# Optimization experiments

Hardware: AMD Instinct MI355X
Metric: run time of the kernel (lower is better)

Reference implementation:

```python
import math
import jax, jax.numpy as jnp
import numpy as np

B, C, T = 8, 512, 8192
UP, DOWN, UP_K, DOWN_K = 2, 2, 12, 12


def kaiser_sinc_filter1d(cutoff, half_width, kernel_size):
    even = kernel_size % 2 == 0
    half_size = kernel_size // 2
    delta_f = 4 * half_width
    A = 2.285 * (half_size - 1) * math.pi * delta_f + 7.95
    if A > 50.0:
        beta = 0.1102 * (A - 8.7)
    elif A >= 21.0:
        beta = 0.5842 * (A - 21) ** 0.4 + 0.07886 * (A - 21.0)
    else:
        beta = 0.0
    window = np.kaiser(kernel_size, beta)
    if even:
        time = np.arange(-half_size, half_size) + 0.5
    else:
        time = np.arange(kernel_size) - half_size
    filt = 2 * cutoff * window * np.sinc(2 * cutoff * time)
    filt = filt / filt.sum()
    return jnp.asarray(filt, dtype=jnp.float32)


def setup_inputs() -> dict:
    key = jax.random.key(0)
    k1, k2, k3 = jax.random.split(key, 3)
    x = jax.random.normal(k1, (B, C, T), dtype=jnp.float32)
    alpha = 0.1 * jax.random.normal(k2, (1, C, 1), dtype=jnp.float32)
    beta = 0.1 * jax.random.normal(k3, (1, C, 1), dtype=jnp.float32)
    up_filter = kaiser_sinc_filter1d(0.5 / UP, 0.6 / UP, UP_K)      # [UP_K]
    down_filter = kaiser_sinc_filter1d(0.5 / DOWN, 0.6 / DOWN, DOWN_K)  # [DOWN_K]
    return {"x": x, "alpha": alpha, "beta": beta,
            "up_filter": up_filter, "down_filter": down_filter}


def _depthwise_kernel(filt, channels):
    # [k] -> [C, 1, k] depthwise kernel (OIH layout)
    return jnp.broadcast_to(filt[None, None, :], (channels, 1, filt.shape[0]))


def _upsample(x, filt, ratio, k):
    # replicate pad, depthwise conv_transpose (via lhs dilation), trim edges
    c = x.shape[1]
    pad = k // ratio - 1
    pad_left = pad * ratio + (k - ratio) // 2
    pad_right = pad * ratio + (k - ratio + 1) // 2
    xp = jnp.pad(x, ((0, 0), (0, 0), (pad, pad)), mode='edge')
    # conv_transpose == conv with flipped kernel, input dilated by stride,
    # full padding (k-1) on each side
    w = _depthwise_kernel(filt[::-1], c)
    y = ratio * jax.lax.conv_general_dilated(
        xp, w, window_strides=(1,), padding=[(k - 1, k - 1)],
        lhs_dilation=(ratio,), feature_group_count=c,
        dimension_numbers=('NCH', 'OIH', 'NCH'))
    return y[..., pad_left:-pad_right]  # [B, C, T*ratio]


def _downsample(x, filt, ratio, k):
    # replicate-pad low-pass depthwise conv with stride=ratio
    c = x.shape[1]
    even = k % 2 == 0
    pad_left = k // 2 - int(even)
    pad_right = k // 2
    xp = jnp.pad(x, ((0, 0), (0, 0), (pad_left, pad_right)), mode='edge')
    w = _depthwise_kernel(filt, c)
    return jax.lax.conv_general_dilated(
        xp, w, window_strides=(ratio,), padding='VALID',
        feature_group_count=c, dimension_numbers=('NCH', 'OIH', 'NCH'))


def _snake_beta(x, alpha, beta):
    a = jnp.exp(alpha)
    b = jnp.exp(beta)
    s = jnp.sin(x * a)
    return x + (s * s) / (b + 1e-9)


def reference(x, alpha, beta, up_filter, down_filter):
    y = _upsample(x, up_filter, UP, UP_K)        # [B, C, T*UP]
    y = _snake_beta(y, alpha, beta)
    y = _downsample(y, down_filter, DOWN, DOWN_K)  # [B, C, T]
    return y
```

## Files before the change

kernel.cpp:

```cpp
#include <hip/hip_runtime.h>
#include <hip/hip_bf16.h>

typedef float v2f __attribute__((ext_vector_type(2)));

namespace {
constexpr int T_LEN = 8192;
constexpr int C_CH  = 512;
constexpr int B_SZ  = 8;
constexpr int TILE  = 2048;
constexpr int NTH   = 256;
constexpr int TPR   = T_LEN / TILE;
constexpr int NS    = TILE + 6;
constexpr int XOFF  = 8;
constexpr int XSZ   = XOFF + TILE + 8;
constexpr int ZSZ   = 2 * TILE + 12;
}

__global__ __launch_bounds__(NTH)
void aaa_fused(const float* __restrict__ x,
               const float* __restrict__ alpha,
               const float* __restrict__ beta,
               const float* __restrict__ upf,
               const float* __restrict__ dnf,
               float* __restrict__ out)
{
    __shared__ __align__(16) float xs[XSZ];
    __shared__ __align__(16) float zs[ZSZ];

    const int tid  = threadIdx.x;
    const int bid  = blockIdx.x;
    const int tile = bid & (TPR - 1);
    const int row  = bid / TPR;
    const int ch   = row & (C_CH - 1);
    const int n0   = tile * TILE;

    const float* __restrict__ xr = x + (size_t)row * T_LEN;
    float* __restrict__ outr     = out + (size_t)row * T_LEN;

    const float av  = expf(alpha[ch]);
    const float rb  = 1.0f / (expf(beta[ch]) + 1e-9f);
    const float avp = av * 0.3183098861837907f;
    const float hrb = 0.5f * rb;

    float cE[6], cO[6];
#pragma unroll
    for (int i = 0; i < 6; ++i) {
        cE[i] = 2.0f * upf[11 - 2 * i];
        cO[i] = 2.0f * upf[10 - 2 * i];
    }
    v2f w[7];
    w[0] = v2f{0.0f, dnf[0]};
#pragma unroll
    for (int k = 1; k < 6; ++k) w[k] = v2f{dnf[2 * k - 1], dnf[2 * k]};
    w[6] = v2f{dnf[11], 0.0f};

    {
        const float4* __restrict__ xr4 = reinterpret_cast<const float4*>(xr + n0);
        float4* xs4 = reinterpret_cast<float4*>(xs + XOFF);
        xs4[tid]       = xr4[tid];
        xs4[tid + NTH] = xr4[tid + NTH];
        if (tid < 6) {
            int gl = max(n0 - 6 + tid, 0);
            xs[XOFF - 6 + tid] = xr[gl];
            int gr = min(n0 + TILE + tid, T_LEN - 1);
            xs[XOFF + TILE + tid] = xr[gr];
        }
    }
    __syncthreads();

    for (int si = tid; si < NS; si += NTH) {
        const float x0 = xs[si + 2];
        const float x1 = xs[si + 3];
        const float x2 = xs[si + 4];
        const float x3 = xs[si + 5];
        const float x4 = xs[si + 6];
        const float x5 = xs[si + 7];
        const float x6 = xs[si + 8];
        float ye = cE[0]*x0 + cE[1]*x1 + cE[2]*x2 + cE[3]*x3 + cE[4]*x4 + cE[5]*x5;
        float yo = cO[0]*x1 + cO[1]*x2 + cO[2]*x3 + cO[3]*x4 + cO[4]*x5 + cO[5]*x6;
        float ue = ye * avp;  ue -= floorf(ue);
        float uo = yo * avp;  uo -= floorf(uo);
        const float ce = __builtin_amdgcn_cosf(ue);
        const float co = __builtin_amdgcn_cosf(uo);
        const float z0 = (ye + hrb) - hrb * ce;
        const float z1 = (yo + hrb) - hrb * co;
        reinterpret_cast<v2f*>(zs)[si] = v2f{z0, z1};
    }
    __syncthreads();

    const v2f* __restrict__ zs2 = reinterpret_cast<const v2f*>(zs);
#pragma unroll
    for (int k = 0; k < TILE / NTH; ++k) {
        const int ln = tid + k * NTH;
        const int n  = n0 + ln;
        if (n >= 3 && n <= T_LEN - 4) {
            v2f acc = w[0] * zs2[ln];
#pragma unroll
            for (int j = 1; j < 7; ++j) acc += w[j] * zs2[ln + j];
            outr[n] = acc.x + acc.y;
        } else {
            const int m0 = 2 * n0 - 6;
            float acc = 0.0f;
#pragma unroll
            for (int j = 0; j < 12; ++j) {
                int m = 2 * n - 5 + j;
                m = min(max(m, 0), 2 * T_LEN - 1);
                const float fj = (j & 1) ? w[(j + 1) >> 1].x : w[j >> 1].y;
                acc += fj * zs[m - m0];
            }
            outr[n] = acc;
        }
    }
}

extern "C" void kernel_launch(void* const* d_in, const int* in_sizes, int n_in,
                              void* d_out, int out_size, void* d_ws, size_t ws_size,
                              hipStream_t stream)
{
    (void)in_sizes; (void)n_in; (void)out_size; (void)d_ws; (void)ws_size;
    const float* x     = (const float*)d_in[0];
    const float* alpha = (const float*)d_in[1];
    const float* beta  = (const float*)d_in[2];
    const float* upf   = (const float*)d_in[3];
    const float* dnf   = (const float*)d_in[4];
    float* out = (float*)d_out;

    dim3 grid(B_SZ * C_CH * TPR);
    dim3 block(NTH);
    aaa_fused<<<grid, block, 0, stream>>>(x, alpha, beta, upf, dnf, out);
}
```

Before: 234.0 us.

## Compute each output run per thread in registers, dropping shared memory staging

Each thread now loads a 32-sample window of x directly from global memory with float4 loads and computes 16 consecutive outputs entirely in registers, so the LDS staging and both block barriers are gone. Edge handling at the row boundaries is moved into explicit folded-coefficient formulas instead of per-sample clamping. The cost is halo recomputation: each thread evaluates 22 upsampled pairs to produce 16 outputs, which adds about 38% redundant snake work and overlapping global reads. Register pressure is also higher, and the per-thread strided float4 accesses may coalesce less well.

```diff
diff --git a/kernel.cpp b/kernel.cpp
--- a/kernel.cpp
+++ b/kernel.cpp
@@ -1,5 +1,4 @@
 #include <hip/hip_runtime.h>
-#include <hip/hip_bf16.h>
 
 typedef float v2f __attribute__((ext_vector_type(2)));
 
@@ -7,13 +6,11 @@
 constexpr int T_LEN = 8192;
 constexpr int C_CH  = 512;
 constexpr int B_SZ  = 8;
-constexpr int TILE  = 2048;
+constexpr int RPT   = 16;
 constexpr int NTH   = 256;
+constexpr int TILE  = RPT * NTH;
 constexpr int TPR   = T_LEN / TILE;
-constexpr int NS    = TILE + 6;
-constexpr int XOFF  = 8;
-constexpr int XSZ   = XOFF + TILE + 8;
-constexpr int ZSZ   = 2 * TILE + 12;
+constexpr int NZP   = RPT + 6;
 }
 
 __global__ __launch_bounds__(NTH)
@@ -24,15 +21,12 @@
                const float* __restrict__ dnf,
                float* __restrict__ out)
 {
-    __shared__ __align__(16) float xs[XSZ];
-    __shared__ __align__(16) float zs[ZSZ];
-
     const int tid  = threadIdx.x;
     const int bid  = blockIdx.x;
     const int tile = bid & (TPR - 1);
-    const int row  = bid / TPR;
+    const int row  = bid >> 1;
     const int ch   = row & (C_CH - 1);
-    const int n0   = tile * TILE;
+    const int Nl   = tile * TILE + tid * RPT;
 
     const float* __restrict__ xr = x + (size_t)row * T_LEN;
     float* __restrict__ outr     = out + (size_t)row * T_LEN;
@@ -54,63 +48,89 @@
     for (int k = 1; k < 6; ++k) w[k] = v2f{dnf[2 * k - 1], dnf[2 * k]};
     w[6] = v2f{dnf[11], 0.0f};
 
-    {
-        const float4* __restrict__ xr4 = reinterpret_cast<const float4*>(xr + n0);
-        float4* xs4 = reinterpret_cast<float4*>(xs + XOFF);
-        xs4[tid]       = xr4[tid];
-        xs4[tid + NTH] = xr4[tid + NTH];
-        if (tid < 6) {
-            int gl = max(n0 - 6 + tid, 0);
-            xs[XOFF - 6 + tid] = xr[gl];
-            int gr = min(n0 + TILE + tid, T_LEN - 1);
-            xs[XOFF + TILE + tid] = xr[gr];
+    float xw[32];
+    if (Nl != 0 && Nl != T_LEN - RPT) {
+        const float4* __restrict__ p4 = reinterpret_cast<const float4*>(xr + Nl - 8);
+#pragma unroll
+        for (int q = 0; q < 8; ++q) {
+            const float4 v = p4[q];
+            xw[4 * q + 0] = v.x; xw[4 * q + 1] = v.y;
+            xw[4 * q + 2] = v.z; xw[4 * q + 3] = v.w;
+        }
+    } else {
+#pragma unroll
+        for (int i = 0; i < 32; ++i) {
+            int g = Nl - 8 + i;
+            g = min(max(g, 0), T_LEN - 1);
+            xw[i] = xr[g];
         }
     }
-    __syncthreads();
 
-    for (int si = tid; si < NS; si += NTH) {
-        const float x0 = xs[si + 2];
-        const float x1 = xs[si + 3];
-        const float x2 = xs[si + 4];
-        const float x3 = xs[si + 5];
-        const float x4 = xs[si + 6];
-        const float x5 = xs[si + 7];
-        const float x6 = xs[si + 8];
-        float ye = cE[0]*x0 + cE[1]*x1 + cE[2]*x2 + cE[3]*x3 + cE[4]*x4 + cE[5]*x5;
-        float yo = cO[0]*x1 + cO[1]*x2 + cO[2]*x3 + cO[3]*x4 + cO[4]*x5 + cO[5]*x6;
+    v2f zp[NZP];
+#pragma unroll
+    for (int si = 0; si < NZP; ++si) {
+        const float x0 = xw[si + 2];
+        const float x1 = xw[si + 3];
+        const float x2 = xw[si + 4];
+        const float x3 = xw[si + 5];
+        const float x4 = xw[si + 6];
+        const float x5 = xw[si + 7];
+        const float x6 = xw[si + 8];
+        const float ye = cE[0]*x0 + cE[1]*x1 + cE[2]*x2 + cE[3]*x3 + cE[4]*x4 + cE[5]*x5;
+        const float yo = cO[0]*x1 + cO[1]*x2 + cO[2]*x3 + cO[3]*x4 + cO[4]*x5 + cO[5]*x6;
         float ue = ye * avp;  ue -= floorf(ue);
         float uo = yo * avp;  uo -= floorf(uo);
         const float ce = __builtin_amdgcn_cosf(ue);
         const float co = __builtin_amdgcn_cosf(uo);
-        const float z0 = (ye + hrb) - hrb * ce;
-        const float z1 = (yo + hrb) - hrb * co;
-        reinterpret_cast<v2f*>(zs)[si] = v2f{z0, z1};
+        zp[si] = v2f{(ye + hrb) - hrb * ce, (yo + hrb) - hrb * co};
     }
-    __syncthreads();
 
-    const v2f* __restrict__ zs2 = reinterpret_cast<const v2f*>(zs);
+    float o[RPT];
 #pragma unroll
-    for (int k = 0; k < TILE / NTH; ++k) {
-        const int ln = tid + k * NTH;
-        const int n  = n0 + ln;
-        if (n >= 3 && n <= T_LEN - 4) {
-            v2f acc = w[0] * zs2[ln];
+    for (int nn = 0; nn < RPT; ++nn) {
+        v2f acc = w[0] * zp[nn];
 #pragma unroll
-            for (int j = 1; j < 7; ++j) acc += w[j] * zs2[ln + j];
-            outr[n] = acc.x + acc.y;
-        } else {
-            const int m0 = 2 * n0 - 6;
-            float acc = 0.0f;
+        for (int k = 1; k < 7; ++k) acc += w[k] * zp[nn + k];
+        o[nn] = acc.x + acc.y;
+    }
+
+    if (Nl == 0) {
+        const float d0=w[0].y, d1=w[1].x, d2=w[1].y, d3=w[2].x, d4=w[2].y, d5=w[3].x,
+                    d6=w[3].y, d7=w[4].x, d8=w[4].y, d9=w[5].x, d10=w[5].y, d11=w[6].x;
+        o[0] = (d0+d1+d2+d3+d4+d5)*zp[3].x + d6*zp[3].y + d7*zp[4].x + d8*zp[4].y
+             + d9*zp[5].x + d10*zp[5].y + d11*zp[6].x;
+        o[1] = (d0+d1+d2+d3)*zp[3].x + d4*zp[3].y + d5*zp[4].x + d6*zp[4].y
+             + d7*zp[5].x + d8*zp[5].y + d9*zp[6].x + d10*zp[6].y + d11*zp[7].x;
+        o[2] = (d0+d1)*zp[3].x + d2*zp[3].y + d3*zp[4].x + d4*zp[4].y + d5*zp[5].x
+             + d6*zp[5].y + d7*zp[6].x + d8*zp[6].y + d9*zp[7].x + d10*zp[7].y
+             + d11*zp[8].x;
+    }
+    if (Nl == T_LEN - RPT) {
+        const float d7=w[4].x, d8=w[4].y, d9=w[5].x, d10=w[5].y, d11=w[6].x;
+        {
+            v2f acc = w[0] * zp[13];
 #pragma unroll
-            for (int j = 0; j < 12; ++j) {
-                int m = 2 * n - 5 + j;
-                m = min(max(m, 0), 2 * T_LEN - 1);
-                const float fj = (j & 1) ? w[(j + 1) >> 1].x : w[j >> 1].y;
-                acc += fj * zs[m - m0];
-            }
-            outr[n] = acc;
+            for (int k = 1; k < 6; ++k) acc += w[k] * zp[13 + k];
+            o[13] = acc.x + acc.y + d11 * zp[18].y;
+        }
+        {
+            v2f acc = w[0] * zp[14];
+#pragma unroll
+            for (int k = 1; k < 5; ++k) acc += w[k] * zp[14 + k];
+            o[14] = acc.x + acc.y + (d9 + d10 + d11) * zp[18].y;
+        }
+        {
+            v2f acc = w[0] * zp[15];
+#pragma unroll
+            for (int k = 1; k < 4; ++k) acc += w[k] * zp[15 + k];
+            o[15] = acc.x + acc.y + (d7 + d8 + d9 + d10 + d11) * zp[18].y;
         }
     }
+
+    float4* __restrict__ po = reinterpret_cast<float4*>(outr + Nl);
+#pragma unroll
+    for (int q = 0; q < 4; ++q)
+        po[q] = float4{o[4*q + 0], o[4*q + 1], o[4*q + 2], o[4*q + 3]};
 }
 
 extern "C" void kernel_launch(void* const* d_in, const int* in_sizes, int n_in,
```

Result: slower. 240.3 us (+2.7%).
